# Kernel optimization log

Measured on AMD Instinct MI355X. Metric: run time of the kernel, lower is better.

Reference implementation:

```python
import jax, jax.numpy as jnp
import numpy as np

H = 16       # query heads
KV = 4       # kv heads
BASE = 10000.0


def _rope(seq_len, head_dim, dtype):
    inv_freq = 1.0 / (BASE ** (jnp.arange(0, head_dim, 2, dtype=jnp.float32) / head_dim))
    t = jnp.arange(seq_len, dtype=jnp.float32)
    freqs = jnp.einsum('i,j->ij', t, inv_freq)          # [S, D/2]
    emb = jnp.concatenate([freqs, freqs], axis=-1)      # [S, D]
    return jnp.cos(emb).astype(dtype), jnp.sin(emb).astype(dtype)


def _rotate_half(x):
    x1, x2 = jnp.split(x, 2, axis=-1)
    return jnp.concatenate([-x2, x1], axis=-1)


def setup_inputs() -> dict:
    key = jax.random.key(0)
    ks = jax.random.split(key, 5)
    B, S, E = 2, 2048, 1024
    return {
        'x': jax.random.normal(ks[0], (B, S, E), jnp.float32),
        'wq': jax.random.normal(ks[1], (E, E), jnp.float32) * (E ** -0.5),
        'wk': jax.random.normal(ks[2], (KV * (E // H), E), jnp.float32) * (E ** -0.5),
        'wv': jax.random.normal(ks[3], (KV * (E // H), E), jnp.float32) * (E ** -0.5),
        'wo': jax.random.normal(ks[4], (E, E), jnp.float32) * (E ** -0.5),
    }


def reference(x, wq, wk, wv, wo):
    B, S, E = x.shape
    D = E // H
    G = H // KV  # query heads per kv head
    scale = D ** -0.5

    q = (x @ wq.T).reshape(B, S, H, D).transpose(0, 2, 1, 3)    # [B,H,S,D]
    k = (x @ wk.T).reshape(B, S, KV, D).transpose(0, 2, 1, 3)   # [B,KV,S,D]
    v = (x @ wv.T).reshape(B, S, KV, D).transpose(0, 2, 1, 3)   # [B,KV,S,D]

    cos, sin = _rope(S, D, x.dtype)                              # [S,D] each
    q = q * cos + _rotate_half(q) * sin
    k = k * cos + _rotate_half(k) * sin

    # GQA: group query heads per kv head instead of materializing repeated K/V
    qg = q.reshape(B, KV, G, S, D)
    scores = jnp.einsum('bkgsd,bktd->bkgst', qg, k) * scale      # [B,KV,G,S,S]
    causal = jnp.triu(jnp.ones((S, S), dtype=bool), k=1)
    scores = jnp.where(causal, jnp.finfo(scores.dtype).min, scores)
    attn = jax.nn.softmax(scores, axis=-1)
    out = jnp.einsum('bkgst,bktd->bkgsd', attn, v)               # [B,KV,G,S,D]
    out = out.reshape(B, H, S, D).transpose(0, 2, 1, 3).reshape(B, S, E)
    return out @ wo.T
```

## Files before the change

kernel.cpp:

```cpp
#include <hip/hip_runtime.h>
#include <stdint.h>

typedef unsigned short u16;
typedef __attribute__((ext_vector_type(8))) short s16x8;
typedef __attribute__((ext_vector_type(4))) float f32x4;
typedef __attribute__((ext_vector_type(4))) unsigned short u16x4;
typedef __attribute__((ext_vector_type(2))) unsigned int u32x2;


__device__ __forceinline__ u16 f2bf(float f) {
  unsigned u = __float_as_uint(f);
  unsigned r = (u + 0x7fffu + ((u >> 16) & 1u)) >> 16;
  return (u16)r;
}
__device__ __forceinline__ unsigned cvt_pk(float lo, float hi) {
  unsigned r;
  asm("v_cvt_pk_bf16_f32 %0, %1, %2" : "=v"(r) : "v"(lo), "v"(hi));
  return r;
}
__device__ __forceinline__ float exp2fast(float x) {
  return __builtin_amdgcn_exp2f(x);
}

typedef const __attribute__((address_space(1))) unsigned int* gas_ptr;
typedef __attribute__((address_space(3))) unsigned int* las_ptr;

__device__ __forceinline__ void g2l16(const void* g, void* l) {
  __builtin_amdgcn_global_load_lds((gas_ptr)g, (las_ptr)l, 16, 0, 0);
}

__device__ __forceinline__ void cvt4(const float* __restrict__ in, u16* __restrict__ out) {
  const f32x4 v = *(const f32x4*)in;
  u16x4 o;
  o[0] = f2bf(v[0]); o[1] = f2bf(v[1]); o[2] = f2bf(v[2]); o[3] = f2bf(v[3]);
  *(u16x4*)out = o;
}


__global__ void prep_kernel(const float* __restrict__ x,  const float* __restrict__ wq,
                            const float* __restrict__ wk, const float* __restrict__ wv,
                            const float* __restrict__ wo,
                            u16* __restrict__ xb, u16* __restrict__ wcat, u16* __restrict__ wob,
                            float* __restrict__ cosT, float* __restrict__ sinT) {
  const long id = (long)blockIdx.x * 256 + threadIdx.x;
  if (id < 262144) {
    cvt4(wq + id * 4, wcat + id * 4);
  } else if (id < 327680) {
    const long i = id - 262144;
    cvt4(wk + i * 4, wcat + 1048576 + i * 4);
  } else if (id < 393216) {
    const long i = id - 327680;
    cvt4(wv + i * 4, wcat + 1310720 + i * 4);
  } else if (id < 655360) {
    const long i = id - 393216;
    cvt4(wo + i * 4, wob + i * 4);
  } else if (id < 671744) {
    const long t = id - 655360;
#pragma unroll
    for (int u = 0; u < 4; ++u) {
      const long idx = t * 4 + u;
      const int s = (int)(idx >> 5), j = (int)(idx & 31);
      const double invd = exp(-(double)j * 0.2878231366242558);
      const float a = (float)s * (float)invd;
      cosT[idx] = cosf(a);
      sinT[idx] = sinf(a);
    }
  } else {
    const long i = id - 671744;
    cvt4(x + i * 4, xb + i * 4);
  }
}


__global__ __launch_bounds__(256, 2) void gemm_qkv_kernel(
    const u16* __restrict__ A, const u16* __restrict__ W,
    u16* __restrict__ qo, u16* __restrict__ ko, u16* __restrict__ vto,
    const float* __restrict__ cosT, const float* __restrict__ sinT) {
  const int K = 1024;
  __shared__ __align__(16) u16 As[128 * 64];
  __shared__ __align__(16) u16 Bs[128 * 64];
  const int tid = threadIdx.x;
  const int lane = tid & 63;
  const int wave = tid >> 6;
  const int g = lane >> 4, l15 = lane & 15;
  const int wr = wave >> 1, wc = wave & 1;
  const long arow0 = (long)blockIdx.x * 128;
  const long wrow0 = (long)blockIdx.y * 128;
  const u16* Ab = A + arow0 * K;
  const u16* Wb = W + wrow0 * K;

  f32x4 acc[4][4] = {};

  for (int k0 = 0; k0 < K; k0 += 64) {
    __syncthreads();
#pragma unroll
    for (int i = 0; i < 4; ++i) {
      const int lbase = i * 256 + wave * 64;
      const int c = lbase + lane;
      const int r = c >> 3, c8 = c & 7;
      g2l16(Ab + (long)r * K + k0 + c8 * 8, (char*)As + lbase * 16);
      g2l16(Wb + (long)r * K + k0 + c8 * 8, (char*)Bs + lbase * 16);
    }
    __syncthreads();
#pragma unroll
    for (int ks = 0; ks < 2; ++ks) {
      s16x8 af[4], bfr[4];
#pragma unroll
      for (int m = 0; m < 4; ++m)
        af[m] = *(const s16x8*)&As[(wr * 64 + m * 16 + l15) * 64 + ks * 32 + g * 8];
#pragma unroll
      for (int n = 0; n < 4; ++n)
        bfr[n] = *(const s16x8*)&Bs[(wc * 64 + n * 16 + l15) * 64 + ks * 32 + g * 8];
      __builtin_amdgcn_s_setprio(1);
#pragma unroll
      for (int m = 0; m < 4; ++m)
#pragma unroll
        for (int n = 0; n < 4; ++n)
          acc[m][n] = __builtin_amdgcn_mfma_f32_16x16x32_bf16(af[m], bfr[n], acc[m][n], 0, 0, 0);
      __builtin_amdgcn_s_setprio(0);
    }
  }

  const int colBase = (int)wrow0 + wc * 64;
  const int j0 = l15;
  const float QSCALE = 0.18033688011112042f;

  if (colBase < 1024) {
    const int h2 = colBase >> 6;
#pragma unroll
    for (int m = 0; m < 4; ++m) {
      const int grow = (int)arow0 + wr * 64 + m * 16 + g * 4;
#pragma unroll
      for (int r = 0; r < 4; ++r) {
        const int row = grow + r;
        const int s = row & 2047, bb = row >> 11;
        const long ob = (((long)(bb * 16 + h2)) * 2048 + s) * 64;
        const float c0 = cosT[s * 32 + j0],      s0 = sinT[s * 32 + j0];
        const float c1 = cosT[s * 32 + 16 + j0], s1 = sinT[s * 32 + 16 + j0];
        qo[ob + j0]      = f2bf((acc[m][0][r] * c0 - acc[m][2][r] * s0) * QSCALE);
        qo[ob + 16 + j0] = f2bf((acc[m][1][r] * c1 - acc[m][3][r] * s1) * QSCALE);
        qo[ob + 32 + j0] = f2bf((acc[m][2][r] * c0 + acc[m][0][r] * s0) * QSCALE);
        qo[ob + 48 + j0] = f2bf((acc[m][3][r] * c1 + acc[m][1][r] * s1) * QSCALE);
      }
    }
  } else if (colBase < 1280) {
    const int kvh2 = (colBase - 1024) >> 6;
#pragma unroll
    for (int m = 0; m < 4; ++m) {
      const int grow = (int)arow0 + wr * 64 + m * 16 + g * 4;
#pragma unroll
      for (int r = 0; r < 4; ++r) {
        const int row = grow + r;
        const int s = row & 2047, bb = row >> 11;
        const long ob = (((long)(bb * 4 + kvh2)) * 2048 + s) * 64;
        const float c0 = cosT[s * 32 + j0],      s0 = sinT[s * 32 + j0];
        const float c1 = cosT[s * 32 + 16 + j0], s1 = sinT[s * 32 + 16 + j0];
        ko[ob + j0]      = f2bf(acc[m][0][r] * c0 - acc[m][2][r] * s0);
        ko[ob + 16 + j0] = f2bf(acc[m][1][r] * c1 - acc[m][3][r] * s1);
        ko[ob + 32 + j0] = f2bf(acc[m][2][r] * c0 + acc[m][0][r] * s0);
        ko[ob + 48 + j0] = f2bf(acc[m][3][r] * c1 + acc[m][1][r] * s1);
      }
    }
  } else {
    const int kvh2 = (colBase - 1280) >> 6;
#pragma unroll
    for (int m = 0; m < 4; ++m) {
      const int grow = (int)arow0 + wr * 64 + m * 16 + g * 4;
#pragma unroll
      for (int r = 0; r < 4; ++r) {
        const int row = grow + r;
        const int s = row & 2047, bb = row >> 11;
#pragma unroll
        for (int n = 0; n < 4; ++n) {
          const int d = n * 16 + j0;
          vto[(((long)(bb * 4 + kvh2)) * 64 + d) * 2048 + s] = f2bf(acc[m][n][r]);
        }
      }
    }
  }
}


__global__ __launch_bounds__(256, 2) void gemm_out_kernel(
    const u16* __restrict__ A, const u16* __restrict__ W, float* __restrict__ Y) {
  const int K = 1024, N = 1024;
  __shared__ __align__(16) u16 As[128 * 64];
  __shared__ __align__(16) u16 Bs[128 * 64];
  const int tid = threadIdx.x;
  const int lane = tid & 63;
  const int wave = tid >> 6;
  const int g = lane >> 4, l15 = lane & 15;
  const int wr = wave >> 1, wc = wave & 1;
  const long arow0 = (long)blockIdx.x * 128;
  const long wrow0 = (long)blockIdx.y * 128;
  const u16* Ab = A + arow0 * K;
  const u16* Wb = W + wrow0 * K;

  f32x4 acc[4][4] = {};

  for (int k0 = 0; k0 < K; k0 += 64) {
    __syncthreads();
#pragma unroll
    for (int i = 0; i < 4; ++i) {
      const int lbase = i * 256 + wave * 64;
      const int c = lbase + lane;
      const int r = c >> 3, c8 = c & 7;
      g2l16(Ab + (long)r * K + k0 + c8 * 8, (char*)As + lbase * 16);
      g2l16(Wb + (long)r * K + k0 + c8 * 8, (char*)Bs + lbase * 16);
    }
    __syncthreads();
#pragma unroll
    for (int ks = 0; ks < 2; ++ks) {
      s16x8 af[4], bfr[4];
#pragma unroll
      for (int m = 0; m < 4; ++m)
        af[m] = *(const s16x8*)&As[(wr * 64 + m * 16 + l15) * 64 + ks * 32 + g * 8];
#pragma unroll
      for (int n = 0; n < 4; ++n)
        bfr[n] = *(const s16x8*)&Bs[(wc * 64 + n * 16 + l15) * 64 + ks * 32 + g * 8];
      __builtin_amdgcn_s_setprio(1);
#pragma unroll
      for (int m = 0; m < 4; ++m)
#pragma unroll
        for (int n = 0; n < 4; ++n)
          acc[m][n] = __builtin_amdgcn_mfma_f32_16x16x32_bf16(af[m], bfr[n], acc[m][n], 0, 0, 0);
      __builtin_amdgcn_s_setprio(0);
    }
  }

#pragma unroll
  for (int m = 0; m < 4; ++m)
#pragma unroll
    for (int n = 0; n < 4; ++n) {
      const long gr0 = arow0 + wr * 64 + m * 16 + g * 4;
      const long gc = wrow0 + wc * 64 + n * 16 + l15;
#pragma unroll
      for (int r = 0; r < 4; ++r)
        Y[(gr0 + r) * N + gc] = acc[m][n][r];
    }
}


__global__ __launch_bounds__(256, 2) void flash_kernel(
    const u16* __restrict__ qg,
    const u16* __restrict__ kg,
    const u16* __restrict__ vtg,
    u16* __restrict__ og) {
  const int tid = threadIdx.x, lane = tid & 63, w = tid >> 6;
  const int g = lane >> 4, l15 = lane & 15;

  const int bid = blockIdx.x;
  const int lid = (bid & 7) * 64 + (bid >> 3);
  const int pr = lid & 15, h = (lid >> 4) & 15, b = lid >> 8;
  const int kvh = h >> 2;

  __shared__ __align__(16) u16 Kl[2][64 * 64];
  __shared__ __align__(16) u16 Vl[2][64 * 64];
  __shared__ __align__(16) u16 Pl[4][16][72];

  const u16* Kp = kg  + ((long)(b * 4 + kvh)) * 2048 * 64;
  const u16* Vp = vtg + ((long)(b * 4 + kvh)) * 64 * 2048;

  auto STAGE = [&](int buf, int kt) {
#pragma unroll
    for (int j = 0; j < 2; ++j) {
      const int lbase = j * 256 + w * 64;
      const int c = lbase + lane;
      const int row = c >> 3, c8 = c & 7;
      const int cs = (c8 ^ (row & 7)) * 8;
      g2l16(Kp + ((long)(kt * 64 + row)) * 64 + cs, (char*)Kl[buf] + lbase * 16);
      g2l16(Vp + (long)row * 2048 + kt * 64 + cs,  (char*)Vl[buf] + lbase * 16);
    }
  };

#pragma unroll 1
  for (int pass = 0; pass < 2; ++pass) {
    const int qt = pass ? (31 - pr) : pr;
    const u16* Qp = qg + (((long)(b * 16 + h)) * 2048 + qt * 64 + w * 16) * 64;
    const s16x8 qf0 = *(const s16x8*)(Qp + l15 * 64 + g * 8);
    const s16x8 qf1 = *(const s16x8*)(Qp + l15 * 64 + 32 + g * 8);

    f32x4 of[4] = {};
    float m = -1e30f, lsum = 0.f;
    const int qrow = qt * 64 + w * 16 + l15;

    int cur = 0;
    STAGE(0, 0);

#pragma unroll 1
    for (int kt = 0; kt <= qt; ++kt) {
      if (kt < qt) {
        STAGE(cur ^ 1, kt + 1);
        asm volatile("s_waitcnt vmcnt(4)" ::: "memory");
      } else {
        asm volatile("s_waitcnt vmcnt(0)" ::: "memory");
      }
      __builtin_amdgcn_s_barrier();
      const u16* Kb = Kl[cur];
      const u16* Vb = Vl[cur];

      f32x4 sf[4] = {};
      __builtin_amdgcn_s_setprio(1);
#pragma unroll
      for (int ks = 0; ks < 2; ++ks) {
        const s16x8 qv = ks ? qf1 : qf0;
#pragma unroll
        for (int fn = 0; fn < 4; ++fn) {
          const int row = fn * 16 + l15;
          const s16x8 kf = *(const s16x8*)((const char*)Kb + row * 128 + (((ks * 4 + g) ^ (row & 7)) << 4));
          sf[fn] = __builtin_amdgcn_mfma_f32_16x16x32_bf16(kf, qv, sf[fn], 0, 0, 0);
        }
      }
      __builtin_amdgcn_s_setprio(0);

      const bool diag = (kt == qt);
      float p[16];
#pragma unroll
      for (int fn = 0; fn < 4; ++fn)
#pragma unroll
        for (int r = 0; r < 4; ++r) {
          float sv = sf[fn][r];
          if (diag) {
            const int kv = kt * 64 + fn * 16 + 4 * g + r;
            if (kv > qrow) sv = -1e30f;
          }
          p[fn * 4 + r] = sv;
        }
      const float t0 = fmaxf(fmaxf(p[0], p[1]), p[2]);
      const float t1 = fmaxf(fmaxf(p[3], p[4]), p[5]);
      const float t2 = fmaxf(fmaxf(p[6], p[7]), p[8]);
      const float t3 = fmaxf(fmaxf(p[9], p[10]), p[11]);
      const float t4 = fmaxf(fmaxf(p[12], p[13]), p[14]);
      float mx = fmaxf(fmaxf(fmaxf(t0, t1), t2), fmaxf(fmaxf(t3, t4), p[15]));
      mx = fmaxf(mx, __shfl_xor(mx, 16));
      mx = fmaxf(mx, __shfl_xor(mx, 32));

      if (!__all(mx - m <= 11.0f)) {
        const float mn = fmaxf(m, mx);
        const float al = exp2fast(m - mn);
        m = mn;
        lsum *= al;
        float alq[4];
#pragma unroll
        for (int r = 0; r < 4; ++r) alq[r] = __shfl(al, 4 * g + r);
#pragma unroll
        for (int fd = 0; fd < 4; ++fd)
#pragma unroll
          for (int r = 0; r < 4; ++r) of[fd][r] *= alq[r];
      }

#pragma unroll
      for (int i = 0; i < 16; ++i) p[i] = exp2fast(p[i] - m);
      const float s0 = (p[0] + p[1]) + (p[2] + p[3]);
      const float s1 = (p[4] + p[5]) + (p[6] + p[7]);
      const float s2 = (p[8] + p[9]) + (p[10] + p[11]);
      const float s3 = (p[12] + p[13]) + (p[14] + p[15]);
      float rs = (s0 + s1) + (s2 + s3);
      rs += __shfl_xor(rs, 16);
      rs += __shfl_xor(rs, 32);
      lsum += rs;

      u16* Pw = &Pl[w][l15][0];
#pragma unroll
      for (int fn = 0; fn < 4; ++fn) {
        const u32x2 v2 = {cvt_pk(p[fn * 4 + 0], p[fn * 4 + 1]),
                          cvt_pk(p[fn * 4 + 2], p[fn * 4 + 3])};
        *(u32x2*)(Pw + fn * 16 + g * 4) = v2;
      }

      __builtin_amdgcn_s_setprio(1);
#pragma unroll
      for (int ks = 0; ks < 2; ++ks) {
        const s16x8 pa = *(const s16x8*)(&Pl[w][l15][ks * 32 + g * 8]);
#pragma unroll
        for (int fd = 0; fd < 4; ++fd) {
          const int vrow = fd * 16 + l15;
          const s16x8 vf = *(const s16x8*)((const char*)Vb + vrow * 128 + (((ks * 4 + g) ^ (vrow & 7)) << 4));
          of[fd] = __builtin_amdgcn_mfma_f32_16x16x32_bf16(pa, vf, of[fd], 0, 0, 0);
        }
      }
      __builtin_amdgcn_s_setprio(0);

      __builtin_amdgcn_s_barrier();
      cur ^= 1;
    }

    float linv[4];
#pragma unroll
    for (int r = 0; r < 4; ++r) linv[r] = 1.0f / __shfl(lsum, 4 * g + r);
    const long orow0 = (long)b * 2048 + qt * 64 + w * 16 + 4 * g;
#pragma unroll
    for (int r = 0; r < 4; ++r) {
      const long gb = (orow0 + r) * 1024 + h * 64;
#pragma unroll
      for (int fd = 0; fd < 4; ++fd)
        og[gb + fd * 16 + l15] = f2bf(of[fd][r] * linv[r]);
    }
  }
}


extern "C" void kernel_launch(void* const* d_in, const int* in_sizes, int n_in,
                              void* d_out, int out_size, void* d_ws, size_t ws_size,
                              hipStream_t stream) {
  (void)in_sizes; (void)n_in; (void)out_size; (void)ws_size;
  const float* x  = (const float*)d_in[0];
  const float* wq = (const float*)d_in[1];
  const float* wk = (const float*)d_in[2];
  const float* wv = (const float*)d_in[3];
  const float* wo = (const float*)d_in[4];
  float* out = (float*)d_out;

  char* p = (char*)d_ws;
  auto alloc = [&](size_t bytes) { char* r = p; p += (bytes + 255) & ~(size_t)255; return r; };

  u16* xb    = (u16*)alloc(4096ull * 1024 * 2);
  u16* wcat  = (u16*)alloc(1536ull * 1024 * 2);
  u16* wob   = (u16*)alloc(1024ull * 1024 * 2);
  u16* qrb   = (u16*)alloc(4096ull * 1024 * 2);
  u16* krb   = (u16*)alloc(4096ull * 256 * 2);
  u16* vtb   = (u16*)alloc(4096ull * 256 * 2);
  u16* aob   = (u16*)alloc(4096ull * 1024 * 2);
  float* cosT = (float*)alloc(2048ull * 32 * 4);
  float* sinT = (float*)alloc(2048ull * 32 * 4);

  prep_kernel<<<6720, 256, 0, stream>>>(x, wq, wk, wv, wo, xb, wcat, wob, cosT, sinT);

  gemm_qkv_kernel<<<dim3(32, 12), 256, 0, stream>>>(xb, wcat, qrb, krb, vtb, cosT, sinT);

  flash_kernel<<<512, 256, 0, stream>>>(qrb, krb, vtb, aob);

  gemm_out_kernel<<<dim3(32, 8), 256, 0, stream>>>(aob, wob, out);
}
```

Measured before the change: 174.7 us.

## Double-buffer GEMM LDS tiles with XOR swizzle and transposed V epilogue

```diff
diff --git a/kernel.cpp b/kernel.cpp
--- a/kernel.cpp
+++ b/kernel.cpp
@@ -77,8 +77,8 @@
     u16* __restrict__ qo, u16* __restrict__ ko, u16* __restrict__ vto,
     const float* __restrict__ cosT, const float* __restrict__ sinT) {
   const int K = 1024;
-  __shared__ __align__(16) u16 As[128 * 64];
-  __shared__ __align__(16) u16 Bs[128 * 64];
+  __shared__ __align__(16) u16 As[2][128 * 64];
+  __shared__ __align__(16) u16 Bs[2][128 * 64];
   const int tid = threadIdx.x;
   const int lane = tid & 63;
   const int wave = tid >> 6;
@@ -88,37 +88,63 @@
   const long wrow0 = (long)blockIdx.y * 128;
   const u16* Ab = A + arow0 * K;
   const u16* Wb = W + wrow0 * K;
-
-  f32x4 acc[4][4] = {};
-
-  for (int k0 = 0; k0 < K; k0 += 64) {
-    __syncthreads();
+  const bool isV = (blockIdx.y >= 10);
+
+  auto STAGE = [&](int buf, int k0) {
 #pragma unroll
     for (int i = 0; i < 4; ++i) {
       const int lbase = i * 256 + wave * 64;
       const int c = lbase + lane;
       const int r = c >> 3, c8 = c & 7;
-      g2l16(Ab + (long)r * K + k0 + c8 * 8, (char*)As + lbase * 16);
-      g2l16(Wb + (long)r * K + k0 + c8 * 8, (char*)Bs + lbase * 16);
-    }
-    __syncthreads();
+      const int cs = (c8 ^ (r & 7)) * 8;
+      g2l16(Ab + (long)r * K + k0 + cs, (char*)As[buf] + lbase * 16);
+      g2l16(Wb + (long)r * K + k0 + cs, (char*)Bs[buf] + lbase * 16);
+    }
+  };
+
+  f32x4 acc[4][4] = {};
+  int cur = 0;
+  STAGE(0, 0);
+
+  for (int k0 = 0; k0 < K; k0 += 64) {
+    if (k0 + 64 < K) {
+      STAGE(cur ^ 1, k0 + 64);
+      asm volatile("s_waitcnt vmcnt(8)" ::: "memory");
+    } else {
+      asm volatile("s_waitcnt vmcnt(0)" ::: "memory");
+    }
+    __builtin_amdgcn_s_barrier();
 #pragma unroll
     for (int ks = 0; ks < 2; ++ks) {
       s16x8 af[4], bfr[4];
 #pragma unroll
-      for (int m = 0; m < 4; ++m)
-        af[m] = *(const s16x8*)&As[(wr * 64 + m * 16 + l15) * 64 + ks * 32 + g * 8];
-#pragma unroll
-      for (int n = 0; n < 4; ++n)
-        bfr[n] = *(const s16x8*)&Bs[(wc * 64 + n * 16 + l15) * 64 + ks * 32 + g * 8];
+      for (int m = 0; m < 4; ++m) {
+        const int row = wr * 64 + m * 16 + l15;
+        af[m] = *(const s16x8*)((const char*)As[cur] + row * 128 + (((ks * 4 + g) ^ (row & 7)) << 4));
+      }
+#pragma unroll
+      for (int n = 0; n < 4; ++n) {
+        const int row = wc * 64 + n * 16 + l15;
+        bfr[n] = *(const s16x8*)((const char*)Bs[cur] + row * 128 + (((ks * 4 + g) ^ (row & 7)) << 4));
+      }
       __builtin_amdgcn_s_setprio(1);
-#pragma unroll
-      for (int m = 0; m < 4; ++m)
-#pragma unroll
-        for (int n = 0; n < 4; ++n)
-          acc[m][n] = __builtin_amdgcn_mfma_f32_16x16x32_bf16(af[m], bfr[n], acc[m][n], 0, 0, 0);
+      if (!isV) {
+#pragma unroll
+        for (int m = 0; m < 4; ++m)
+#pragma unroll
+          for (int n = 0; n < 4; ++n)
+            acc[m][n] = __builtin_amdgcn_mfma_f32_16x16x32_bf16(af[m], bfr[n], acc[m][n], 0, 0, 0);
+      } else {
+#pragma unroll
+        for (int m = 0; m < 4; ++m)
+#pragma unroll
+          for (int n = 0; n < 4; ++n)
+            acc[m][n] = __builtin_amdgcn_mfma_f32_16x16x32_bf16(bfr[m], af[n], acc[m][n], 0, 0, 0);
+      }
       __builtin_amdgcn_s_setprio(0);
     }
+    __builtin_amdgcn_s_barrier();
+    cur ^= 1;
   }
 
   const int colBase = (int)wrow0 + wc * 64;
@@ -163,18 +189,18 @@
     }
   } else {
     const int kvh2 = (colBase - 1280) >> 6;
-#pragma unroll
-    for (int m = 0; m < 4; ++m) {
-      const int grow = (int)arow0 + wr * 64 + m * 16 + g * 4;
+    const int bb = (int)(arow0 >> 11);
+    const int sBase = (int)(arow0 & 2047) + wr * 64;
+    const long vrow0 = ((long)(bb * 4 + kvh2)) * 64;
+#pragma unroll
+    for (int mw = 0; mw < 4; ++mw) {
+      const int d0 = mw * 16 + g * 4;
 #pragma unroll
       for (int r = 0; r < 4; ++r) {
-        const int row = grow + r;
-        const int s = row & 2047, bb = row >> 11;
-#pragma unroll
-        for (int n = 0; n < 4; ++n) {
-          const int d = n * 16 + j0;
-          vto[(((long)(bb * 4 + kvh2)) * 64 + d) * 2048 + s] = f2bf(acc[m][n][r]);
-        }
+        const long db = (vrow0 + d0 + r) * 2048;
+#pragma unroll
+        for (int nx = 0; nx < 4; ++nx)
+          vto[db + sBase + nx * 16 + l15] = f2bf(acc[mw][nx][r]);
       }
     }
   }
@@ -184,8 +210,8 @@
 __global__ __launch_bounds__(256, 2) void gemm_out_kernel(
     const u16* __restrict__ A, const u16* __restrict__ W, float* __restrict__ Y) {
   const int K = 1024, N = 1024;
-  __shared__ __align__(16) u16 As[128 * 64];
-  __shared__ __align__(16) u16 Bs[128 * 64];
+  __shared__ __align__(16) u16 As[2][128 * 64];
+  __shared__ __align__(16) u16 Bs[2][128 * 64];
   const int tid = threadIdx.x;
   const int lane = tid & 63;
   const int wave = tid >> 6;
@@ -196,28 +222,43 @@
   const u16* Ab = A + arow0 * K;
   const u16* Wb = W + wrow0 * K;
 
-  f32x4 acc[4][4] = {};
-
-  for (int k0 = 0; k0 < K; k0 += 64) {
-    __syncthreads();
+  auto STAGE = [&](int buf, int k0) {
 #pragma unroll
     for (int i = 0; i < 4; ++i) {
       const int lbase = i * 256 + wave * 64;
       const int c = lbase + lane;
       const int r = c >> 3, c8 = c & 7;
-      g2l16(Ab + (long)r * K + k0 + c8 * 8, (char*)As + lbase * 16);
-      g2l16(Wb + (long)r * K + k0 + c8 * 8, (char*)Bs + lbase * 16);
-    }
-    __syncthreads();
+      const int cs = (c8 ^ (r & 7)) * 8;
+      g2l16(Ab + (long)r * K + k0 + cs, (char*)As[buf] + lbase * 16);
+      g2l16(Wb + (long)r * K + k0 + cs, (char*)Bs[buf] + lbase * 16);
+    }
+  };
+
+  f32x4 acc[4][4] = {};
+  int cur = 0;
+  STAGE(0, 0);
+
+  for (int k0 = 0; k0 < K; k0 += 64) {
+    if (k0 + 64 < K) {
+      STAGE(cur ^ 1, k0 + 64);
+      asm volatile("s_waitcnt vmcnt(8)" ::: "memory");
+    } else {
+      asm volatile("s_waitcnt vmcnt(0)" ::: "memory");
+    }
+    __builtin_amdgcn_s_barrier();
 #pragma unroll
     for (int ks = 0; ks < 2; ++ks) {
       s16x8 af[4], bfr[4];
 #pragma unroll
-      for (int m = 0; m < 4; ++m)
-        af[m] = *(const s16x8*)&As[(wr * 64 + m * 16 + l15) * 64 + ks * 32 + g * 8];
-#pragma unroll
-      for (int n = 0; n < 4; ++n)
-        bfr[n] = *(const s16x8*)&Bs[(wc * 64 + n * 16 + l15) * 64 + ks * 32 + g * 8];
+      for (int m = 0; m < 4; ++m) {
+        const int row = wr * 64 + m * 16 + l15;
+        af[m] = *(const s16x8*)((const char*)As[cur] + row * 128 + (((ks * 4 + g) ^ (row & 7)) << 4));
+      }
+#pragma unroll
+      for (int n = 0; n < 4; ++n) {
+        const int row = wc * 64 + n * 16 + l15;
+        bfr[n] = *(const s16x8*)((const char*)Bs[cur] + row * 128 + (((ks * 4 + g) ^ (row & 7)) << 4));
+      }
       __builtin_amdgcn_s_setprio(1);
 #pragma unroll
       for (int m = 0; m < 4; ++m)
@@ -226,6 +267,8 @@
           acc[m][n] = __builtin_amdgcn_mfma_f32_16x16x32_bf16(af[m], bfr[n], acc[m][n], 0, 0, 0);
       __builtin_amdgcn_s_setprio(0);
     }
+    __builtin_amdgcn_s_barrier();
+    cur ^= 1;
   }
 
 #pragma unroll
```

Result: faster. 168.2 us (-3.7%).
